# Kernel tuning notes

Measured on AMD Instinct MI355X. Metric: run time of the kernel, lower is better.

Reference implementation:

```python
import jax, jax.numpy as jnp
import numpy as np

B, C, H, W = 8, 192, 128, 128
NUM_HEADS = 4
EPS = 1e-12  # torch F.normalize default eps
DN = ('NCHW', 'OIHW', 'NCHW')


def setup_inputs() -> dict:
    key = jax.random.key(0)
    k1, k2, k3, k4 = jax.random.split(key, 4)
    x = jax.random.normal(k1, (B, C, H, W), dtype=jnp.float32)
    qkv_w = jax.random.normal(k2, (3 * C, C, 1, 1), dtype=jnp.float32) * 0.05
    dw_w = jax.random.normal(k3, (3 * C, 1, 3, 3), dtype=jnp.float32) * 0.1
    proj_w = jax.random.normal(k4, (C, C, 1, 1), dtype=jnp.float32) * 0.05
    temperature = jnp.ones((NUM_HEADS, 1, 1), dtype=jnp.float32)
    return {"x": x, "qkv_w": qkv_w, "dw_w": dw_w, "proj_w": proj_w,
            "temperature": temperature}


def _l2norm(t):
    # F.normalize(t, dim=-1): divide by max(||t||, eps)
    n = jnp.sqrt(jnp.sum(t * t, axis=-1, keepdims=True))
    return t / jnp.maximum(n, EPS)


def reference(x, qkv_w, dw_w, proj_w, temperature):
    b, c, h, w = x.shape
    nh = NUM_HEADS
    cph = c // nh
    # 1x1 conv -> depthwise 3x3 conv (groups = 3*dim)
    qkv = jax.lax.conv_general_dilated(x, qkv_w, (1, 1), 'VALID',
                                       dimension_numbers=DN)
    qkv = jax.lax.conv_general_dilated(qkv, dw_w, (1, 1), [(1, 1), (1, 1)],
                                       dimension_numbers=DN,
                                       feature_group_count=3 * c)
    q, k, v = jnp.split(qkv, 3, axis=1)
    # [b, nh, cph, h*w]
    q = q.reshape(b, nh, cph, h * w)
    k = k.reshape(b, nh, cph, h * w)
    v = v.reshape(b, nh, cph, h * w)
    q = _l2norm(q)
    k = _l2norm(k)
    # channel attention: [b, nh, cph, cph]
    attn = jnp.einsum('bhcn,bhdn->bhcd', q, k) * temperature
    attn = jax.nn.softmax(attn, axis=-1)
    out = jnp.einsum('bhcd,bhdn->bhcn', attn, v)
    out = out.reshape(b, c, h, w)
    return jax.lax.conv_general_dilated(out, proj_w, (1, 1), 'VALID',
                                        dimension_numbers=DN)
```

## Files before the change

kernel.cpp:

```cpp
#include <hip/hip_runtime.h>
#include <hip/hip_bf16.h>

typedef __hip_bfloat16 bf16;
typedef __attribute__((ext_vector_type(8))) __bf16 bf16x8;
typedef __attribute__((ext_vector_type(4))) float f32x4;

#define HW 16384

static __device__ __forceinline__ float b2f(bf16 v) { return __bfloat162float(v); }
static __device__ __forceinline__ bf16 f2b(float v) { return __float2bfloat16(v); }
static __device__ __forceinline__ float blo(unsigned int w) {
    return __uint_as_float(w << 16);
}
static __device__ __forceinline__ float bhi(unsigned int w) {
    return __uint_as_float(w & 0xffff0000u);
}
static __device__ __forceinline__ unsigned short f2bu(float v) {
    union { bf16 b; unsigned short u; } c; c.b = f2b(v); return c.u;
}

static __device__ __forceinline__ void stf(float* p, float v) { *p = v; }
static __device__ __forceinline__ void stf(bf16* p, float v)  { *p = f2b(v); }

static __device__ __forceinline__ void load8(const float* p, float* v) {
    const float4* q = (const float4*)p;
    float4 a = q[0], b = q[1];
    v[0] = a.x; v[1] = a.y; v[2] = a.z; v[3] = a.w;
    v[4] = b.x; v[5] = b.y; v[6] = b.z; v[7] = b.w;
}
static __device__ __forceinline__ void load8(const bf16* p, float* v) {
    uint4 u = *(const uint4*)p;
    v[0] = blo(u.x); v[1] = bhi(u.x); v[2] = blo(u.y); v[3] = bhi(u.y);
    v[4] = blo(u.z); v[5] = bhi(u.z); v[6] = blo(u.w); v[7] = bhi(u.w);
}

template <typename TX, typename TY>
__global__ __launch_bounds__(256) void gemm_mfma(
    const float* __restrict__ Wm, const TX* __restrict__ X,
    TY* __restrict__ Y, int M, int K, int N)
{
    const int mb = blockIdx.x, nb = blockIdx.y, b = blockIdx.z;
    const TX* Xb = X + (size_t)b * K * N;
    TY* Yb = Y + (size_t)b * M * N;
    const int m0 = mb * 64, n0 = nb * 64;

    __shared__ __bf16 As[64][40];
    __shared__ __bf16 Bs[64][40];

    const int tid = threadIdx.x;
    const int lane = tid & 63, wave = tid >> 6;
    const int wm = (wave & 1) * 32, wn = (wave >> 1) * 32;
    const int r16 = lane & 15, quad = lane >> 4;

    f32x4 acc[2][2];
#pragma unroll
    for (int i = 0; i < 2; i++)
#pragma unroll
        for (int j = 0; j < 2; j++) acc[i][j] = (f32x4){0.f, 0.f, 0.f, 0.f};

    for (int k0 = 0; k0 < K; k0 += 32) {
        {
            int m = tid >> 2, kq = (tid & 3) * 8;
            float v[8];
            load8(Wm + (size_t)(m0 + m) * K + k0 + kq, v);
            bf16x8 pk;
#pragma unroll
            for (int j = 0; j < 8; j++) pk[j] = (__bf16)v[j];
            *(bf16x8*)&As[m][kq] = pk;
        }
        {
            int k = tid >> 3, n8 = (tid & 7) * 8;
            float v[8];
            load8(Xb + (size_t)(k0 + k) * N + n0 + n8, v);
#pragma unroll
            for (int j = 0; j < 8; j++) Bs[n8 + j][k] = (__bf16)v[j];
        }
        __syncthreads();
        bf16x8 a0 = *(const bf16x8*)&As[wm + r16][quad * 8];
        bf16x8 a1 = *(const bf16x8*)&As[wm + 16 + r16][quad * 8];
        bf16x8 b0 = *(const bf16x8*)&Bs[wn + r16][quad * 8];
        bf16x8 b1 = *(const bf16x8*)&Bs[wn + 16 + r16][quad * 8];
        acc[0][0] = __builtin_amdgcn_mfma_f32_16x16x32_bf16(a0, b0, acc[0][0], 0, 0, 0);
        acc[0][1] = __builtin_amdgcn_mfma_f32_16x16x32_bf16(a0, b1, acc[0][1], 0, 0, 0);
        acc[1][0] = __builtin_amdgcn_mfma_f32_16x16x32_bf16(a1, b0, acc[1][0], 0, 0, 0);
        acc[1][1] = __builtin_amdgcn_mfma_f32_16x16x32_bf16(a1, b1, acc[1][1], 0, 0, 0);
        __syncthreads();
    }

#pragma unroll
    for (int sm = 0; sm < 2; sm++)
#pragma unroll
        for (int sn = 0; sn < 2; sn++) {
            int gr = m0 + wm + sm * 16 + quad * 4;
            int gc = n0 + wn + sn * 16 + r16;
#pragma unroll
            for (int r = 0; r < 4; r++)
                stf(Yb + (size_t)(gr + r) * N + gc, acc[sm][sn][r]);
        }
}

__global__ __launch_bounds__(256) void dwconv3x3(
    const bf16* __restrict__ in, const float* __restrict__ wdw,
    bf16* __restrict__ out)
{
    const int plane = blockIdx.x >> 2;
    const int ybase = (blockIdx.x & 3) << 5;
    const int c = plane % 576;
    const bf16* ip = in + ((size_t)plane << 14);

    __shared__ unsigned short Ls[34][128];

    for (int i = threadIdx.x; i < 34 * 16; i += 256) {
        int r = i >> 4, cx = i & 15;
        int y = ybase - 1 + r;
        uint4 v = make_uint4(0u, 0u, 0u, 0u);
        if (y >= 0 && y < 128) v = ((const uint4*)(ip + ((size_t)y << 7)))[cx];
        ((uint4*)Ls[r])[cx] = v;
    }

    float w[9];
#pragma unroll
    for (int i = 0; i < 9; i++) w[i] = wdw[c * 9 + i];

    __syncthreads();

    const int lr = threadIdx.x >> 3;
    const int c0 = (threadIdx.x & 7) << 4;

    float row[3][18];
#pragma unroll
    for (int r3 = 0; r3 < 3; r3++) {
        int rr = lr + r3;
        row[r3][0]  = c0 ? blo((unsigned int)Ls[rr][c0 - 1] << 0) * 0.f + __uint_as_float((unsigned int)Ls[rr][c0 - 1] << 16) : 0.f;
        row[r3][17] = (c0 + 16 < 128) ? __uint_as_float((unsigned int)Ls[rr][c0 + 16] << 16) : 0.f;
        const uint4* rp = (const uint4*)&Ls[rr][c0];
        uint4 p0 = rp[0], p1 = rp[1];
        row[r3][1] = blo(p0.x); row[r3][2] = bhi(p0.x);
        row[r3][3] = blo(p0.y); row[r3][4] = bhi(p0.y);
        row[r3][5] = blo(p0.z); row[r3][6] = bhi(p0.z);
        row[r3][7] = blo(p0.w); row[r3][8] = bhi(p0.w);
        row[r3][9]  = blo(p1.x); row[r3][10] = bhi(p1.x);
        row[r3][11] = blo(p1.y); row[r3][12] = bhi(p1.y);
        row[r3][13] = blo(p1.z); row[r3][14] = bhi(p1.z);
        row[r3][15] = blo(p1.w); row[r3][16] = bhi(p1.w);
    }

    union { unsigned short s[16]; uint4 v[2]; } o;
#pragma unroll
    for (int j = 0; j < 16; j++) {
        float s = 0.f;
#pragma unroll
        for (int r3 = 0; r3 < 3; r3++)
            s += w[r3 * 3 + 0] * row[r3][j] + w[r3 * 3 + 1] * row[r3][j + 1]
               + w[r3 * 3 + 2] * row[r3][j + 2];
        o.s[j] = f2bu(s);
    }
    uint4* op = (uint4*)(out + ((size_t)plane << 14) + ((size_t)(ybase + lr) << 7) + c0);
    op[0] = o.v[0];
    op[1] = o.v[1];
}

__global__ __launch_bounds__(256) void rownorm(
    const bf16* __restrict__ qkv, float* __restrict__ rn)
{
    int r = blockIdx.x;
    int which = (r >= 1536) ? 1 : 0;
    int rr = r - which * 1536;
    int b = rr / 192, c = rr % 192;
    const bf16* p = qkv + ((size_t)(b * 576 + which * 192 + c) << 14);

    float s = 0.f;
    for (int i = threadIdx.x * 8; i < HW; i += 256 * 8) {
        float v[8];
        load8(p + i, v);
#pragma unroll
        for (int j = 0; j < 8; j++) s += v[j] * v[j];
    }
#pragma unroll
    for (int off = 32; off; off >>= 1) s += __shfl_down(s, off);
    __shared__ float red[4];
    if ((threadIdx.x & 63) == 0) red[threadIdx.x >> 6] = s;
    __syncthreads();
    if (threadIdx.x == 0) {
        float t = red[0] + red[1] + red[2] + red[3];
        rn[r] = 1.0f / fmaxf(sqrtf(t), 1e-12f);
    }
}

__global__ __launch_bounds__(256) void attn_dots(
    const bf16* __restrict__ qkv, float* __restrict__ attn)
{
    const int bh = blockIdx.y, b = bh >> 2, h = bh & 3;
    const int n0 = blockIdx.x * 1024;
    const bf16* q  = qkv + ((size_t)(b * 576 + h * 48) << 14);
    const bf16* kp = qkv + ((size_t)(b * 576 + 192 + h * 48) << 14);

    __shared__ float qt[48][68];
    __shared__ float kt[48][68];

    const int tid = threadIdx.x;
    const int cg = tid >> 4, dg = tid & 15;

    float acc[3][3] = {{0.f, 0.f, 0.f}, {0.f, 0.f, 0.f}, {0.f, 0.f, 0.f}};

    for (int s0 = 0; s0 < 1024; s0 += 64) {
        for (int i = tid; i < 48 * 8; i += 256) {
            int rowi = i / 8, cx = (i & 7) * 8;
            size_t off = ((size_t)rowi << 14) + n0 + s0 + cx;
            float v[8];
            load8(q + off, v);
#pragma unroll
            for (int j = 0; j < 8; j++) qt[rowi][cx + j] = v[j];
            load8(kp + off, v);
#pragma unroll
            for (int j = 0; j < 8; j++) kt[rowi][cx + j] = v[j];
        }
        __syncthreads();
#pragma unroll 8
        for (int n = 0; n < 64; n++) {
            float a0 = qt[cg * 3 + 0][n], a1 = qt[cg * 3 + 1][n], a2 = qt[cg * 3 + 2][n];
            float b0 = kt[dg * 3 + 0][n], b1 = kt[dg * 3 + 1][n], b2 = kt[dg * 3 + 2][n];
            acc[0][0] += a0 * b0; acc[0][1] += a0 * b1; acc[0][2] += a0 * b2;
            acc[1][0] += a1 * b0; acc[1][1] += a1 * b1; acc[1][2] += a1 * b2;
            acc[2][0] += a2 * b0; acc[2][1] += a2 * b1; acc[2][2] += a2 * b2;
        }
        __syncthreads();
    }
#pragma unroll
    for (int i = 0; i < 3; i++)
#pragma unroll
        for (int j = 0; j < 3; j++)
            atomicAdd(&attn[(size_t)bh * 2304 + (cg * 3 + i) * 48 + dg * 3 + j],
                      acc[i][j]);
}

__global__ __launch_bounds__(64) void softmax48(
    float* __restrict__ attn, const float* __restrict__ rn,
    const float* __restrict__ temp)
{
    int bh = blockIdx.x, b = bh >> 2, h = bh & 3;
    int c = threadIdx.x;
    if (c >= 48) return;
    float t = temp[h];
    float iq = rn[b * 192 + h * 48 + c];
    const float* ik = rn + 1536 + b * 192 + h * 48;
    float* row = attn + (size_t)bh * 2304 + c * 48;

    float v[48];
    float mx = -1e30f;
#pragma unroll
    for (int d = 0; d < 48; d++) {
        v[d] = row[d] * iq * ik[d] * t;
        mx = fmaxf(mx, v[d]);
    }
    float s = 0.f;
#pragma unroll
    for (int d = 0; d < 48; d++) {
        v[d] = expf(v[d] - mx);
        s += v[d];
    }
    float inv = 1.0f / s;
#pragma unroll
    for (int d = 0; d < 48; d++) row[d] = v[d] * inv;
}

__global__ __launch_bounds__(256) void attn_v(
    const float* __restrict__ attn, const bf16* __restrict__ qkv,
    bf16* __restrict__ outb)
{
    int bh = blockIdx.y, b = bh >> 2, h = bh & 3;
    int n = blockIdx.x * 256 + threadIdx.x;

    __shared__ float A[48 * 48];
    for (int i = threadIdx.x; i < 2304; i += 256) A[i] = attn[(size_t)bh * 2304 + i];
    __syncthreads();

    const bf16* v = qkv + ((size_t)(b * 576 + 384 + h * 48) << 14) + n;
    float acc[48];
#pragma unroll
    for (int c = 0; c < 48; c++) acc[c] = 0.f;

    for (int d = 0; d < 48; d++) {
        float vd = b2f(v[(size_t)d << 14]);
#pragma unroll
        for (int c = 0; c < 48; c++) acc[c] += A[c * 48 + d] * vd;
    }
    bf16* o = outb + ((size_t)(b * 192 + h * 48) << 14) + n;
#pragma unroll
    for (int c = 0; c < 48; c++) o[(size_t)c << 14] = f2b(acc[c]);
}

extern "C" void kernel_launch(void* const* d_in, const int* in_sizes, int n_in,
                              void* d_out, int out_size, void* d_ws, size_t ws_size,
                              hipStream_t stream)
{
    const float* x      = (const float*)d_in[0];
    const float* qkv_w  = (const float*)d_in[1];
    const float* dw_w   = (const float*)d_in[2];
    const float* proj_w = (const float*)d_in[3];
    const float* temp   = (const float*)d_in[4];
    float* out = (float*)d_out;

    char* ws = (char*)d_ws;
    const size_t qkvBytes = (size_t)8 * 576 * HW * sizeof(bf16);
    bf16*  qkv0 = (bf16*)ws;
    bf16*  qkv1 = (bf16*)(ws + qkvBytes);
    float* attn = (float*)(ws + 2 * qkvBytes);
    float* rn   = (float*)(ws + 2 * qkvBytes + (size_t)32 * 2304 * sizeof(float));
    bf16*  aout = qkv0;

    gemm_mfma<float, bf16><<<dim3(9, 256, 8), 256, 0, stream>>>(
        qkv_w, x, qkv0, 576, 192, HW);
    dwconv3x3<<<dim3(8 * 576 * 4), 256, 0, stream>>>(qkv0, dw_w, qkv1);
    rownorm<<<dim3(3072), 256, 0, stream>>>(qkv1, rn);
    hipMemsetAsync(attn, 0, (size_t)32 * 2304 * sizeof(float), stream);
    attn_dots<<<dim3(16, 32), 256, 0, stream>>>(qkv1, attn);
    softmax48<<<dim3(32), 64, 0, stream>>>(attn, rn, temp);
    attn_v<<<dim3(64, 32), 256, 0, stream>>>(attn, qkv1, aout);
    gemm_mfma<bf16, float><<<dim3(3, 256, 8), 256, 0, stream>>>(
        proj_w, aout, out, 192, 192, HW);
}
```

Measured before the change: 559.6 us.

## Restructure 1x1-conv GEMMs: register-resident weights, full-K tiles, prefetch pipeline

The 1x1-conv GEMM kernel now keeps its weight fragments for the whole K=192 in registers. Each block loops over 8 consecutive 64-column tiles, staging the full-K activation tile into an XOR-swizzled shared buffer. Global loads for the next tile are issued before the MFMAs of the current tile run, and the per-32-K double barrier loop is removed. The grid is flattened with batch as the fastest-varying index. This trades higher register and LDS use, and lower occupancy, for less redundant weight traffic and fewer synchronisations. A dead expression in the depthwise conv halo load is also simplified.

New measurement: 680.2 us. 21.6% more time.

```diff
diff --git a/kernel.cpp b/kernel.cpp
--- a/kernel.cpp
+++ b/kernel.cpp
@@ -4,6 +4,7 @@
 typedef __hip_bfloat16 bf16;
 typedef __attribute__((ext_vector_type(8))) __bf16 bf16x8;
 typedef __attribute__((ext_vector_type(4))) float f32x4;
+typedef unsigned int u32;
 
 #define HW 16384
 
@@ -37,66 +38,138 @@
 template <typename TX, typename TY>
 __global__ __launch_bounds__(256) void gemm_mfma(
     const float* __restrict__ Wm, const TX* __restrict__ X,
-    TY* __restrict__ Y, int M, int K, int N)
-{
-    const int mb = blockIdx.x, nb = blockIdx.y, b = blockIdx.z;
+    TY* __restrict__ Y, int MB)
+{
+    constexpr int K = 192, N = HW, T = 8;
+    constexpr int NPF = (sizeof(TX) == 4) ? 16 : 8;
+
+    const int b    = blockIdx.x & 7;
+    const int slot = blockIdx.x >> 3;
+    const int mb   = slot % MB;
+    const int g    = slot / MB;
+    const int m0   = mb * 64;
+
     const TX* Xb = X + (size_t)b * K * N;
-    TY* Yb = Y + (size_t)b * M * N;
-    const int m0 = mb * 64, n0 = nb * 64;
-
-    __shared__ __bf16 As[64][40];
-    __shared__ __bf16 Bs[64][40];
-
-    const int tid = threadIdx.x;
+    TY* Yb = Y + (size_t)b * (MB * 64) * N;
+
+    __shared__ __bf16 Bs[64][256];
+
+    const int tid  = threadIdx.x;
     const int lane = tid & 63, wave = tid >> 6;
     const int wm = (wave & 1) * 32, wn = (wave >> 1) * 32;
     const int r16 = lane & 15, quad = lane >> 4;
 
-    f32x4 acc[2][2];
-#pragma unroll
-    for (int i = 0; i < 2; i++)
-#pragma unroll
-        for (int j = 0; j < 2; j++) acc[i][j] = (f32x4){0.f, 0.f, 0.f, 0.f};
-
-    for (int k0 = 0; k0 < K; k0 += 32) {
-        {
-            int m = tid >> 2, kq = (tid & 3) * 8;
-            float v[8];
-            load8(Wm + (size_t)(m0 + m) * K + k0 + kq, v);
-            bf16x8 pk;
-#pragma unroll
-            for (int j = 0; j < 8; j++) pk[j] = (__bf16)v[j];
-            *(bf16x8*)&As[m][kq] = pk;
-        }
-        {
-            int k = tid >> 3, n8 = (tid & 7) * 8;
-            float v[8];
-            load8(Xb + (size_t)(k0 + k) * N + n0 + n8, v);
-#pragma unroll
-            for (int j = 0; j < 8; j++) Bs[n8 + j][k] = (__bf16)v[j];
-        }
-        __syncthreads();
-        bf16x8 a0 = *(const bf16x8*)&As[wm + r16][quad * 8];
-        bf16x8 a1 = *(const bf16x8*)&As[wm + 16 + r16][quad * 8];
-        bf16x8 b0 = *(const bf16x8*)&Bs[wn + r16][quad * 8];
-        bf16x8 b1 = *(const bf16x8*)&Bs[wn + 16 + r16][quad * 8];
-        acc[0][0] = __builtin_amdgcn_mfma_f32_16x16x32_bf16(a0, b0, acc[0][0], 0, 0, 0);
-        acc[0][1] = __builtin_amdgcn_mfma_f32_16x16x32_bf16(a0, b1, acc[0][1], 0, 0, 0);
-        acc[1][0] = __builtin_amdgcn_mfma_f32_16x16x32_bf16(a1, b0, acc[1][0], 0, 0, 0);
-        acc[1][1] = __builtin_amdgcn_mfma_f32_16x16x32_bf16(a1, b1, acc[1][1], 0, 0, 0);
-        __syncthreads();
-    }
-
-#pragma unroll
-    for (int sm = 0; sm < 2; sm++)
-#pragma unroll
-        for (int sn = 0; sn < 2; sn++) {
-            int gr = m0 + wm + sm * 16 + quad * 4;
-            int gc = n0 + wn + sn * 16 + r16;
-#pragma unroll
-            for (int r = 0; r < 4; r++)
-                stf(Yb + (size_t)(gr + r) * N + gc, acc[sm][sn][r]);
-        }
+    bf16x8 aReg[6][2];
+#pragma unroll
+    for (int ks = 0; ks < 6; ks++)
+#pragma unroll
+        for (int h = 0; h < 2; h++) {
+            const float* ap = Wm + (size_t)(m0 + wm + h * 16 + r16) * K
+                            + ks * 32 + quad * 8;
+            float4 f0 = ((const float4*)ap)[0];
+            float4 f1 = ((const float4*)ap)[1];
+            bf16x8 fr;
+            fr[0] = (__bf16)f0.x; fr[1] = (__bf16)f0.y;
+            fr[2] = (__bf16)f0.z; fr[3] = (__bf16)f0.w;
+            fr[4] = (__bf16)f1.x; fr[5] = (__bf16)f1.y;
+            fr[6] = (__bf16)f1.z; fr[7] = (__bf16)f1.w;
+            aReg[ks][h] = fr;
+        }
+
+    const int kb   = tid >> 3;
+    const int noct = tid & 7;
+    const bool act = (kb < 24);
+
+    uint4 pf[NPF];
+
+    auto load_tile = [&](int t) {
+        if (!act) return;
+        const TX* src = Xb + (size_t)(kb * 8) * N + g * 512 + t * 64 + noct * 8;
+#pragma unroll
+        for (int j = 0; j < 8; j++) {
+            if constexpr (sizeof(TX) == 4) {
+                const uint4* s = (const uint4*)(src + (size_t)j * N);
+                pf[2 * j]     = s[0];
+                pf[2 * j + 1] = s[1];
+            } else {
+                pf[j] = *(const uint4*)(src + (size_t)j * N);
+            }
+        }
+    };
+
+    auto write_tile = [&]() {
+        if (!act) return;
+        char* dst = (char*)Bs + (size_t)(noct * 8) * 512 + ((kb ^ noct) << 4);
+#pragma unroll
+        for (int jn = 0; jn < 8; jn++) {
+            u32 w[4];
+#pragma unroll
+            for (int wd = 0; wd < 4; wd++) {
+                if constexpr (sizeof(TX) == 4) {
+                    float f0 = ((const float*)&pf[4 * wd + (jn >> 2)])[jn & 3];
+                    float f1 = ((const float*)&pf[4 * wd + 2 + (jn >> 2)])[jn & 3];
+                    w[wd] = (u32)f2bu(f0) | ((u32)f2bu(f1) << 16);
+                } else {
+                    u32 a = ((const u32*)&pf[2 * wd])[jn >> 1];
+                    u32 c = ((const u32*)&pf[2 * wd + 1])[jn >> 1];
+                    w[wd] = (jn & 1) ? ((a >> 16) | (c & 0xffff0000u))
+                                     : ((a & 0xffffu) | (c << 16));
+                }
+            }
+            *(uint4*)(dst + jn * 512) = make_uint4(w[0], w[1], w[2], w[3]);
+        }
+    };
+
+    const int nA = wn + r16, nB = wn + 16 + r16;
+    const char* pA = (const char*)Bs + (size_t)nA * 512;
+    const char* pB = (const char*)Bs + (size_t)nB * 512;
+    const int xA = nA >> 3, xB = nB >> 3;
+
+    load_tile(0);
+
+    for (int t = 0; t < T; t++) {
+        asm volatile("" ::: "memory");
+        __builtin_amdgcn_s_barrier();
+        asm volatile("" ::: "memory");
+        __builtin_amdgcn_sched_barrier(0);
+
+        write_tile();
+        if (t + 1 < T) load_tile(t + 1);
+
+        asm volatile("s_waitcnt lgkmcnt(0)" ::: "memory");
+        __builtin_amdgcn_s_barrier();
+        asm volatile("" ::: "memory");
+        __builtin_amdgcn_sched_barrier(0);
+
+        f32x4 acc[2][2];
+#pragma unroll
+        for (int i = 0; i < 2; i++)
+#pragma unroll
+            for (int j = 0; j < 2; j++) acc[i][j] = (f32x4){0.f, 0.f, 0.f, 0.f};
+
+#pragma unroll
+        for (int ks = 0; ks < 6; ks++) {
+            const int kb0 = ks * 4 + quad;
+            bf16x8 b0 = *(const bf16x8*)(pA + ((kb0 ^ xA) << 4));
+            bf16x8 b1 = *(const bf16x8*)(pB + ((kb0 ^ xB) << 4));
+            acc[0][0] = __builtin_amdgcn_mfma_f32_16x16x32_bf16(aReg[ks][0], b0, acc[0][0], 0, 0, 0);
+            acc[1][0] = __builtin_amdgcn_mfma_f32_16x16x32_bf16(aReg[ks][1], b0, acc[1][0], 0, 0, 0);
+            acc[0][1] = __builtin_amdgcn_mfma_f32_16x16x32_bf16(aReg[ks][0], b1, acc[0][1], 0, 0, 0);
+            acc[1][1] = __builtin_amdgcn_mfma_f32_16x16x32_bf16(aReg[ks][1], b1, acc[1][1], 0, 0, 0);
+        }
+
+        const int n0 = g * 512 + t * 64;
+#pragma unroll
+        for (int sm = 0; sm < 2; sm++)
+#pragma unroll
+            for (int sn = 0; sn < 2; sn++) {
+                const int gr = m0 + wm + sm * 16 + quad * 4;
+                const int gc = n0 + wn + sn * 16 + r16;
+#pragma unroll
+                for (int r = 0; r < 4; r++)
+                    stf(Yb + (size_t)(gr + r) * N + gc, acc[sm][sn][r]);
+            }
+    }
 }
 
 __global__ __launch_bounds__(256) void dwconv3x3(
@@ -131,7 +204,7 @@
 #pragma unroll
     for (int r3 = 0; r3 < 3; r3++) {
         int rr = lr + r3;
-        row[r3][0]  = c0 ? blo((unsigned int)Ls[rr][c0 - 1] << 0) * 0.f + __uint_as_float((unsigned int)Ls[rr][c0 - 1] << 16) : 0.f;
+        row[r3][0]  = c0 ? __uint_as_float((unsigned int)Ls[rr][c0 - 1] << 16) : 0.f;
         row[r3][17] = (c0 + 16 < 128) ? __uint_as_float((unsigned int)Ls[rr][c0 + 16] << 16) : 0.f;
         const uint4* rp = (const uint4*)&Ls[rr][c0];
         uint4 p0 = rp[0], p1 = rp[1];
@@ -309,14 +382,14 @@
     float* rn   = (float*)(ws + 2 * qkvBytes + (size_t)32 * 2304 * sizeof(float));
     bf16*  aout = qkv0;
 
-    gemm_mfma<float, bf16><<<dim3(9, 256, 8), 256, 0, stream>>>(
-        qkv_w, x, qkv0, 576, 192, HW);
+    gemm_mfma<float, bf16><<<dim3(9 * 32 * 8), 256, 0, stream>>>(
+        qkv_w, x, qkv0, 9);
     dwconv3x3<<<dim3(8 * 576 * 4), 256, 0, stream>>>(qkv0, dw_w, qkv1);
     rownorm<<<dim3(3072), 256, 0, stream>>>(qkv1, rn);
     hipMemsetAsync(attn, 0, (size_t)32 * 2304 * sizeof(float), stream);
     attn_dots<<<dim3(16, 32), 256, 0, stream>>>(qkv1, attn);
     softmax48<<<dim3(32), 64, 0, stream>>>(attn, rn, temp);
     attn_v<<<dim3(64, 32), 256, 0, stream>>>(attn, qkv1, aout);
-    gemm_mfma<bf16, float><<<dim3(3, 256, 8), 256, 0, stream>>>(
-        proj_w, aout, out, 192, 192, HW);
-}
+    gemm_mfma<bf16, float><<<dim3(3 * 32 * 8), 256, 0, stream>>>(
+        proj_w, aout, out, 3);
+}
```

## Transpose activations to HW-major bf16 and rewrite GEMM to register-resident operands

Applied to the files above, without the earlier changes.

Adds a transpose-and-cast pre-pass so the 1x1-conv GEMM reads the input as contiguous bf16 K-vectors, and pre-casts the weights to bf16. The GEMM is rewritten to load A and B fragments straight from global memory into registers with double buffering and no LDS or barriers, using 64x128 tiles. attn_v now handles all 4 heads per block and writes its output transposed, so the projection GEMM can use the same layout. The cost is an extra transpose kernel and extra global traffic, plus reused workspace regions that must not collide.

Result: slower. 675.0 us (+20.6%).

```diff
diff --git a/kernel.cpp b/kernel.cpp
--- a/kernel.cpp
+++ b/kernel.cpp
@@ -4,6 +4,7 @@
 typedef __hip_bfloat16 bf16;
 typedef __attribute__((ext_vector_type(8))) __bf16 bf16x8;
 typedef __attribute__((ext_vector_type(4))) float f32x4;
+typedef unsigned int u32;
 
 #define HW 16384
 
@@ -34,65 +35,113 @@
     v[4] = blo(u.z); v[5] = bhi(u.z); v[6] = blo(u.w); v[7] = bhi(u.w);
 }
 
-template <typename TX, typename TY>
+__global__ __launch_bounds__(256) void tr_cast(
+    const float* __restrict__ x, bf16* __restrict__ xT)
+{
+    const int b  = blockIdx.x >> 8;
+    const int t  = blockIdx.x & 255;
+    const int hw0 = t << 6;
+    const float* xb = x + (size_t)b * 192 * HW;
+
+    __shared__ unsigned short T[64][200];
+
+    const int tid = threadIdx.x;
+    for (int i = tid; i < 192 * 16; i += 256) {
+        int c = i >> 4, seg = i & 15;
+        float4 f = *(const float4*)(xb + (size_t)c * HW + hw0 + seg * 4);
+        T[seg * 4 + 0][c] = f2bu(f.x);
+        T[seg * 4 + 1][c] = f2bu(f.y);
+        T[seg * 4 + 2][c] = f2bu(f.z);
+        T[seg * 4 + 3][c] = f2bu(f.w);
+    }
+    __syncthreads();
+
+    const int hw = tid >> 2, c0 = (tid & 3) * 48;
+    const uint4* src = (const uint4*)&T[hw][c0];
+    uint4* dst = (uint4*)(xT + ((size_t)(b * HW) + hw0 + hw) * 192 + c0);
+#pragma unroll
+    for (int j = 0; j < 6; j++) dst[j] = src[j];
+}
+
+__global__ __launch_bounds__(256) void wcast(
+    const float* __restrict__ w, bf16* __restrict__ o, int n4)
+{
+    int i = blockIdx.x * 256 + threadIdx.x;
+    if (i < n4) {
+        float4 f = ((const float4*)w)[i];
+        u32 lo = (u32)f2bu(f.x) | ((u32)f2bu(f.y) << 16);
+        u32 hi = (u32)f2bu(f.z) | ((u32)f2bu(f.w) << 16);
+        ((uint2*)o)[i] = make_uint2(lo, hi);
+    }
+}
+
+template <typename TY>
 __global__ __launch_bounds__(256) void gemm_mfma(
-    const float* __restrict__ Wm, const TX* __restrict__ X,
-    TY* __restrict__ Y, int M, int K, int N)
-{
-    const int mb = blockIdx.x, nb = blockIdx.y, b = blockIdx.z;
-    const TX* Xb = X + (size_t)b * K * N;
-    TY* Yb = Y + (size_t)b * M * N;
-    const int m0 = mb * 64, n0 = nb * 64;
-
-    __shared__ __bf16 As[64][40];
-    __shared__ __bf16 Bs[64][40];
-
-    const int tid = threadIdx.x;
+    const bf16* __restrict__ Wb, const bf16* __restrict__ Bx,
+    TY* __restrict__ Y, int MB)
+{
+    constexpr int N = HW;
+    const int b    = blockIdx.x & 7;
+    const int slot = blockIdx.x >> 3;
+    const int mb   = slot % MB;
+    const int ng   = slot / MB;
+    const int m0   = mb * 64;
+    const int n0   = ng * 128;
+
+    const bf16* Bb = Bx + (size_t)b * N * 192;
+    TY* Yb = Y + (size_t)b * (MB * 64) * N;
+
+    const int tid  = threadIdx.x;
     const int lane = tid & 63, wave = tid >> 6;
-    const int wm = (wave & 1) * 32, wn = (wave >> 1) * 32;
+    const int wm = (wave & 1) * 32, wn = (wave >> 1) * 64;
     const int r16 = lane & 15, quad = lane >> 4;
 
-    f32x4 acc[2][2];
+    const bf16* aBase = Wb + (size_t)(m0 + wm + r16) * 192 + quad * 8;
+    bf16x8 aReg[6][2];
+#pragma unroll
+    for (int ks = 0; ks < 6; ks++)
+#pragma unroll
+        for (int h = 0; h < 2; h++)
+            aReg[ks][h] = *(const bf16x8*)(aBase + h * 16 * 192 + ks * 32);
+
+    const bf16* bBase = Bb + (size_t)(n0 + wn + r16) * 192 + quad * 8;
+
+    f32x4 acc[2][4];
 #pragma unroll
     for (int i = 0; i < 2; i++)
 #pragma unroll
-        for (int j = 0; j < 2; j++) acc[i][j] = (f32x4){0.f, 0.f, 0.f, 0.f};
-
-    for (int k0 = 0; k0 < K; k0 += 32) {
-        {
-            int m = tid >> 2, kq = (tid & 3) * 8;
-            float v[8];
-            load8(Wm + (size_t)(m0 + m) * K + k0 + kq, v);
-            bf16x8 pk;
-#pragma unroll
-            for (int j = 0; j < 8; j++) pk[j] = (__bf16)v[j];
-            *(bf16x8*)&As[m][kq] = pk;
-        }
-        {
-            int k = tid >> 3, n8 = (tid & 7) * 8;
-            float v[8];
-            load8(Xb + (size_t)(k0 + k) * N + n0 + n8, v);
-#pragma unroll
-            for (int j = 0; j < 8; j++) Bs[n8 + j][k] = (__bf16)v[j];
-        }
-        __syncthreads();
-        bf16x8 a0 = *(const bf16x8*)&As[wm + r16][quad * 8];
-        bf16x8 a1 = *(const bf16x8*)&As[wm + 16 + r16][quad * 8];
-        bf16x8 b0 = *(const bf16x8*)&Bs[wn + r16][quad * 8];
-        bf16x8 b1 = *(const bf16x8*)&Bs[wn + 16 + r16][quad * 8];
-        acc[0][0] = __builtin_amdgcn_mfma_f32_16x16x32_bf16(a0, b0, acc[0][0], 0, 0, 0);
-        acc[0][1] = __builtin_amdgcn_mfma_f32_16x16x32_bf16(a0, b1, acc[0][1], 0, 0, 0);
-        acc[1][0] = __builtin_amdgcn_mfma_f32_16x16x32_bf16(a1, b0, acc[1][0], 0, 0, 0);
-        acc[1][1] = __builtin_amdgcn_mfma_f32_16x16x32_bf16(a1, b1, acc[1][1], 0, 0, 0);
-        __syncthreads();
+        for (int j = 0; j < 4; j++) acc[i][j] = (f32x4){0.f, 0.f, 0.f, 0.f};
+
+    bf16x8 pb[2][4];
+#pragma unroll
+    for (int sn = 0; sn < 4; sn++) {
+        pb[0][sn] = *(const bf16x8*)(bBase + sn * 16 * 192 + 0 * 32);
+        pb[1][sn] = *(const bf16x8*)(bBase + sn * 16 * 192 + 1 * 32);
+    }
+
+#pragma unroll
+    for (int ks = 0; ks < 6; ks++) {
+        const int par = ks & 1;
+#pragma unroll
+        for (int sn = 0; sn < 4; sn++) {
+            acc[0][sn] = __builtin_amdgcn_mfma_f32_16x16x32_bf16(
+                aReg[ks][0], pb[par][sn], acc[0][sn], 0, 0, 0);
+            acc[1][sn] = __builtin_amdgcn_mfma_f32_16x16x32_bf16(
+                aReg[ks][1], pb[par][sn], acc[1][sn], 0, 0, 0);
+        }
+        if (ks + 2 < 6) {
+#pragma unroll
+            for (int sn = 0; sn < 4; sn++)
+                pb[par][sn] = *(const bf16x8*)(bBase + sn * 16 * 192 + (ks + 2) * 32);
+        }
     }
 
 #pragma unroll
     for (int sm = 0; sm < 2; sm++)
 #pragma unroll
-        for (int sn = 0; sn < 2; sn++) {
-            int gr = m0 + wm + sm * 16 + quad * 4;
-            int gc = n0 + wn + sn * 16 + r16;
+        for (int sn = 0; sn < 4; sn++) {
+            const int gr = m0 + wm + sm * 16 + quad * 4;
+            const int gc = n0 + wn + sn * 16 + r16;
 #pragma unroll
             for (int r = 0; r < 4; r++)
                 stf(Yb + (size_t)(gr + r) * N + gc, acc[sm][sn][r]);
@@ -131,7 +180,7 @@
 #pragma unroll
     for (int r3 = 0; r3 < 3; r3++) {
         int rr = lr + r3;
-        row[r3][0]  = c0 ? blo((unsigned int)Ls[rr][c0 - 1] << 0) * 0.f + __uint_as_float((unsigned int)Ls[rr][c0 - 1] << 16) : 0.f;
+        row[r3][0]  = c0 ? __uint_as_float((unsigned int)Ls[rr][c0 - 1] << 16) : 0.f;
         row[r3][17] = (c0 + 16 < 128) ? __uint_as_float((unsigned int)Ls[rr][c0 + 16] << 16) : 0.f;
         const uint4* rp = (const uint4*)&Ls[rr][c0];
         uint4 p0 = rp[0], p1 = rp[1];
@@ -264,30 +313,39 @@
     for (int d = 0; d < 48; d++) row[d] = v[d] * inv;
 }
 
-__global__ __launch_bounds__(256) void attn_v(
+__global__ __launch_bounds__(256) void attn_v_t(
     const float* __restrict__ attn, const bf16* __restrict__ qkv,
-    bf16* __restrict__ outb)
-{
-    int bh = blockIdx.y, b = bh >> 2, h = bh & 3;
-    int n = blockIdx.x * 256 + threadIdx.x;
-
-    __shared__ float A[48 * 48];
-    for (int i = threadIdx.x; i < 2304; i += 256) A[i] = attn[(size_t)bh * 2304 + i];
+    bf16* __restrict__ outT)
+{
+    const int b = blockIdx.y;
+    const int n = blockIdx.x * 256 + threadIdx.x;
+
+    __shared__ float A4[4][2304];
+    for (int i = threadIdx.x; i < 4 * 2304; i += 256)
+        ((float*)A4)[i] = attn[(size_t)b * 4 * 2304 + i];
     __syncthreads();
 
-    const bf16* v = qkv + ((size_t)(b * 576 + 384 + h * 48) << 14) + n;
-    float acc[48];
-#pragma unroll
-    for (int c = 0; c < 48; c++) acc[c] = 0.f;
-
-    for (int d = 0; d < 48; d++) {
-        float vd = b2f(v[(size_t)d << 14]);
-#pragma unroll
-        for (int c = 0; c < 48; c++) acc[c] += A[c * 48 + d] * vd;
-    }
-    bf16* o = outb + ((size_t)(b * 192 + h * 48) << 14) + n;
-#pragma unroll
-    for (int c = 0; c < 48; c++) o[(size_t)c << 14] = f2b(acc[c]);
+    bf16* o = outT + ((size_t)(b * HW) + n) * 192;
+#pragma unroll 1
+    for (int h = 0; h < 4; h++) {
+        const bf16* v = qkv + ((size_t)(b * 576 + 384 + h * 48) << 14) + n;
+        float acc[48];
+#pragma unroll
+        for (int c = 0; c < 48; c++) acc[c] = 0.f;
+        for (int d = 0; d < 48; d++) {
+            float vd = b2f(v[(size_t)d << 14]);
+#pragma unroll
+            for (int c = 0; c < 48; c++) acc[c] += A4[h][c * 48 + d] * vd;
+        }
+        uint4 pk[6];
+        u32* pw = (u32*)pk;
+#pragma unroll
+        for (int j = 0; j < 24; j++)
+            pw[j] = (u32)f2bu(acc[2 * j]) | ((u32)f2bu(acc[2 * j + 1]) << 16);
+        uint4* d4 = (uint4*)(o + h * 48);
+#pragma unroll
+        for (int j = 0; j < 6; j++) d4[j] = pk[j];
+    }
 }
 
 extern "C" void kernel_launch(void* const* d_in, const int* in_sizes, int n_in,
@@ -307,16 +365,21 @@
     bf16*  qkv1 = (bf16*)(ws + qkvBytes);
     float* attn = (float*)(ws + 2 * qkvBytes);
     float* rn   = (float*)(ws + 2 * qkvBytes + (size_t)32 * 2304 * sizeof(float));
-    bf16*  aout = qkv0;
-
-    gemm_mfma<float, bf16><<<dim3(9, 256, 8), 256, 0, stream>>>(
-        qkv_w, x, qkv0, 576, 192, HW);
+
+    bf16* xT    = (bf16*)qkv1;
+    bf16* aoutT = (bf16*)qkv0;
+    bf16* Wb    = (bf16*)attn;
+    bf16* Pb    = (bf16*)(ws + 100 * 1024 * 1024);
+
+    tr_cast<<<dim3(8 * 256), 256, 0, stream>>>(x, xT);
+    wcast<<<dim3(108), 256, 0, stream>>>(qkv_w, Wb, 27648);
+    gemm_mfma<bf16><<<dim3(8 * 9 * 128), 256, 0, stream>>>(Wb, xT, qkv0, 9);
     dwconv3x3<<<dim3(8 * 576 * 4), 256, 0, stream>>>(qkv0, dw_w, qkv1);
+    wcast<<<dim3(36), 256, 0, stream>>>(proj_w, Pb, 9216);
     rownorm<<<dim3(3072), 256, 0, stream>>>(qkv1, rn);
     hipMemsetAsync(attn, 0, (size_t)32 * 2304 * sizeof(float), stream);
     attn_dots<<<dim3(16, 32), 256, 0, stream>>>(qkv1, attn);
     softmax48<<<dim3(32), 64, 0, stream>>>(attn, rn, temp);
-    attn_v<<<dim3(64, 32), 256, 0, stream>>>(attn, qkv1, aout);
-    gemm_mfma<bf16, float><<<dim3(3, 256, 8), 256, 0, stream>>>(
-        proj_w, aout, out, 192, 192, HW);
-}
+    attn_v_t<<<dim3(64, 8), 256, 0, stream>>>(attn, qkv1, aoutT);
+    gemm_mfma<float><<<dim3(8 * 3 * 128), 256, 0, stream>>>(Pb, aoutT, out, 3);
+}
```
